# Performance work log

Hardware: AMD Instinct MI355X
Metric: run time of the kernel (lower is better)

Reference implementation:

```python
import jax, jax.numpy as jnp
import numpy as np

# Dimensions
T, B, N, E = 16, 16, 1024, 16384   # seq len, graphs per step, nodes/graph, edges/graph
F_IN, MID, H = 128, 16, 256        # node features, GCN mid channels, hidden_dim
RATIO = 0.8
K = int(np.ceil(RATIO * N))        # SAGPooling keeps K=820 nodes per graph


def setup_inputs() -> dict:
    key = jax.random.key(0)
    ks = jax.random.split(key, 16)
    def p(k, shape, s=0.05):
        return jax.random.normal(k, shape, dtype=jnp.float32) * s
    return {
        "x": jax.random.normal(ks[0], (T, B, N, F_IN), dtype=jnp.float32),
        "edge_index": jax.random.randint(ks[1], (T, B, 2, E), 0, N, dtype=jnp.int32),
        "conv1_W": p(ks[2], (F_IN, MID)),
        "conv1_b": p(ks[3], (MID,)),
        "sag_Wl": p(ks[4], (MID, 1)),   # GraphConv lin_rel (neighbor aggregate)
        "sag_Wr": p(ks[5], (MID, 1)),   # GraphConv lin_root (self)
        "sag_b": p(ks[6], (1,)),
        "conv2_W": p(ks[7], (MID, H)),
        "conv2_b": p(ks[8], (H,)),
        "W_ih": p(ks[9], (4 * H, H)),   # LSTM gates in PyTorch order i,f,g,o
        "W_hh": p(ks[10], (4 * H, H)),
        "b_ih": p(ks[11], (4 * H,)),
        "b_hh": p(ks[12], (4 * H,)),
        "cls_W": p(ks[13], (H, 1)),
        "cls_b": p(ks[14], (1,)),
    }


def _gcn(x, src, dst, w, W, b, n):
    # GCNConv with self-loops: out_i = sum_j d_i^-1/2 d_j^-1/2 w_ij (x_j W) + d_i^-1 (x_i W) + b
    h = x @ W                                            # [n, out]
    deg = jnp.ones((n,), x.dtype).at[dst].add(w)         # +1 for self-loop weight
    dinv = jax.lax.rsqrt(deg)
    coef = dinv[src] * dinv[dst] * w                     # [e]
    out = jnp.zeros_like(h).at[dst].add(h[src] * coef[:, None])
    return out + h * (dinv * dinv)[:, None] + b


def _graph_embed(x, ei, conv1_W, conv1_b, sag_Wl, sag_Wr, sag_b, conv2_W, conv2_b):
    src, dst = ei[0], ei[1]
    w = jnp.ones((E,), x.dtype)
    # conv1 + relu
    h1 = jax.nn.relu(_gcn(x, src, dst, w, conv1_W, conv1_b, N))
    # SAGPooling score via GraphConv(16 -> 1): sum-aggregate neighbors + root
    agg = jnp.zeros_like(h1).at[dst].add(h1[src])
    score = (agg @ sag_Wl + h1 @ sag_Wr + sag_b)[:, 0]   # [N]
    sv, perm = jax.lax.top_k(score, K)                   # top-k nodes
    xp = h1[perm] * jnp.tanh(sv)[:, None]                # gate kept nodes
    # remap edges to kept-node ids; drop edges touching removed nodes via zero weight
    newidx = jnp.full((N,), -1, jnp.int32).at[perm].set(jnp.arange(K, dtype=jnp.int32))
    ns, nd = newidx[src], newidx[dst]
    valid = (ns >= 0) & (nd >= 0)
    ew = valid.astype(x.dtype)
    ns = jnp.where(valid, ns, 0)
    nd = jnp.where(valid, nd, 0)
    # conv2 + relu, then global mean pool over the K kept nodes
    h2 = jax.nn.relu(_gcn(xp, ns, nd, ew, conv2_W, conv2_b, K))
    return h2.mean(axis=0)                               # [H]


def reference(x, edge_index, conv1_W, conv1_b, sag_Wl, sag_Wr, sag_b,
              conv2_W, conv2_b, W_ih, W_hh, b_ih, b_hh, cls_W, cls_b):
    embed = lambda xg, eg: _graph_embed(xg, eg, conv1_W, conv1_b,
                                        sag_Wl, sag_Wr, sag_b, conv2_W, conv2_b)
    emb = jax.vmap(jax.vmap(embed))(x, edge_index)       # [T, B, H]

    def step(carry, xt):
        h, c = carry
        g = xt @ W_ih.T + b_ih + h @ W_hh.T + b_hh
        i, f, gg, o = jnp.split(g, 4, axis=-1)
        c = jax.nn.sigmoid(f) * c + jax.nn.sigmoid(i) * jnp.tanh(gg)
        h = jax.nn.sigmoid(o) * jnp.tanh(c)
        return (h, c), None

    h0 = jnp.zeros((B, H), x.dtype)
    (hT, _), _ = jax.lax.scan(step, (h0, h0), emb)       # hT = lstm_out[:, -1, :]
    return hT @ cls_W + cls_b                            # [B, 1]
```

## Files before the change

### kernel.cpp

```cpp
#include <hip/hip_runtime.h>
#include <cmath>

#define TT 16
#define BB 16
#define NN 1024
#define EE 16384
#define FIN 128
#define MIDC 16
#define HH 256
#define KK 820
#define HS 20

#define OFF_HBUF   0
#define N_HBUF     (NN*HS)
#define OFF_CSR    (OFF_HBUF + N_HBUF)
#define N_CSR      (EE/2)
#define OFF_HEAD   (OFF_CSR + N_CSR)
#define OFF_CUR    (OFF_HEAD + NN + 1)
#define OFF_SCANA  (OFF_CUR + NN)
#define OFF_DINV   (OFF_SCANA + NN)
#define OFF_UB     (OFF_DINV + NN)
#define OFF_HIST   (OFF_UB + NN)
#define OFF_S      (OFF_HIST + 256)
#define OFF_WCNT   (OFF_S + 256)
#define OFF_CTRL   (OFF_WCNT + 16)
#define SM_FLOATS  (OFF_CTRL + 8)
#define SM_BYTES   (SM_FLOATS * 4)

__global__ __launch_bounds__(1024) void k_graph(
    const float* __restrict__ x, const int* __restrict__ ei,
    const float* __restrict__ W1, const float* __restrict__ b1,
    const float* __restrict__ Wl, const float* __restrict__ Wr,
    const float* __restrict__ bsag, const float* __restrict__ W2,
    const float* __restrict__ b2, float* __restrict__ emb)
{
  extern __shared__ __align__(16) float sm[];
  float*          hbuf  = sm + OFF_HBUF;
  float4*         hb4   = (float4*)hbuf;
  unsigned short* csr   = (unsigned short*)(sm + OFF_CSR);
  int*            head  = (int*)(sm + OFF_HEAD);
  int*            cur   = (int*)(sm + OFF_CUR);
  float*          dinvb = sm + OFF_DINV;
  unsigned*       ubv   = (unsigned*)(sm + OFF_UB);
  int*            hist  = (int*)(sm + OFF_HIST);
  int*            S     = (int*)(sm + OFF_S);
  int*            wcnt  = (int*)(sm + OFF_WCNT);
  int*            ctrl  = (int*)(sm + OFF_CTRL);

  const int g   = blockIdx.x;
  const int tid = threadIdx.x;
  const float* xg   = x  + (size_t)g * (NN*FIN);
  const int*   srcp = ei + (size_t)g * (2*EE);
  const int*   dstp = srcp + EE;

  cur[tid] = 0;

  float hown[MIDC];
  {
    const float4* xr = (const float4*)(xg + (size_t)tid * FIN);
#pragma unroll
    for (int c = 0; c < MIDC; ++c) hown[c] = 0.0f;
    for (int k4 = 0; k4 < FIN/4; ++k4) {
      float4 v = xr[k4];
      const float* w0 = W1 + (k4*4 + 0)*MIDC;
      const float* w1 = W1 + (k4*4 + 1)*MIDC;
      const float* w2 = W1 + (k4*4 + 2)*MIDC;
      const float* w3 = W1 + (k4*4 + 3)*MIDC;
#pragma unroll
      for (int c = 0; c < MIDC; ++c)
        hown[c] += v.x*w0[c] + v.y*w1[c] + v.z*w2[c] + v.w*w3[c];
    }
    hb4[tid*5+0] = make_float4(hown[0],  hown[1],  hown[2],  hown[3]);
    hb4[tid*5+1] = make_float4(hown[4],  hown[5],  hown[6],  hown[7]);
    hb4[tid*5+2] = make_float4(hown[8],  hown[9],  hown[10], hown[11]);
    hb4[tid*5+3] = make_float4(hown[12], hown[13], hown[14], hown[15]);
  }
  __syncthreads();

  for (int e = tid; e < EE; e += 1024) atomicAdd(&cur[dstp[e]], 1);
  __syncthreads();

  {
    const int lane_ = tid & 63, wid_ = tid >> 6;
    int v = cur[tid];
    int xscan = v;
#pragma unroll
    for (int off = 1; off < 64; off <<= 1) {
      int y = __shfl_up(xscan, off);
      if (lane_ >= off) xscan += y;
    }
    if (lane_ == 63) wcnt[wid_] = xscan;
    __syncthreads();
    if (tid < 64) {
      int w = (tid < 16) ? wcnt[tid] : 0;
#pragma unroll
      for (int off = 1; off < 16; off <<= 1) {
        int y = __shfl_up(w, off);
        if (tid >= off) w += y;
      }
      if (tid < 16) wcnt[tid] = w;
    }
    __syncthreads();
    int ex = xscan - v + ((wid_ == 0) ? 0 : wcnt[wid_ - 1]);
    head[tid] = ex;
    cur[tid]  = ex;
    if (tid == 0) head[NN] = EE;
    dinvb[tid] = rsqrtf((float)(v + 1));
  }
  __syncthreads();

  for (int e = tid; e < EE; e += 1024) {
    int s = srcp[e], d = dstp[e];
    int pos = atomicAdd(&cur[d], 1);
    csr[pos] = (unsigned short)s;
  }
  __syncthreads();

  const int beg = head[tid], end = head[tid+1];

  float h1own[MIDC];
  {
    float accv[MIDC];
#pragma unroll
    for (int c = 0; c < MIDC; ++c) accv[c] = 0.0f;
    for (int p = beg; p < end; ++p) {
      int s = csr[p];
      float ds_ = dinvb[s];
      float4 a0 = hb4[s*5+0], a1 = hb4[s*5+1], a2 = hb4[s*5+2], a3 = hb4[s*5+3];
      accv[0]  += a0.x*ds_; accv[1]  += a0.y*ds_; accv[2]  += a0.z*ds_; accv[3]  += a0.w*ds_;
      accv[4]  += a1.x*ds_; accv[5]  += a1.y*ds_; accv[6]  += a1.z*ds_; accv[7]  += a1.w*ds_;
      accv[8]  += a2.x*ds_; accv[9]  += a2.y*ds_; accv[10] += a2.z*ds_; accv[11] += a2.w*ds_;
      accv[12] += a3.x*ds_; accv[13] += a3.y*ds_; accv[14] += a3.z*ds_; accv[15] += a3.w*ds_;
    }
    float di = dinvb[tid];
#pragma unroll
    for (int c = 0; c < MIDC; ++c)
      h1own[c] = fmaxf(di*accv[c] + hown[c]*di*di + b1[c], 0.0f);
  }
  __syncthreads();
  hb4[tid*5+0] = make_float4(h1own[0],  h1own[1],  h1own[2],  h1own[3]);
  hb4[tid*5+1] = make_float4(h1own[4],  h1own[5],  h1own[6],  h1own[7]);
  hb4[tid*5+2] = make_float4(h1own[8],  h1own[9],  h1own[10], h1own[11]);
  hb4[tid*5+3] = make_float4(h1own[12], h1own[13], h1own[14], h1own[15]);
  __syncthreads();

  float score;
  unsigned myu;
  {
    float aggv[MIDC];
#pragma unroll
    for (int c = 0; c < MIDC; ++c) aggv[c] = 0.0f;
    for (int p = beg; p < end; ++p) {
      int s = csr[p];
      float4 a0 = hb4[s*5+0], a1 = hb4[s*5+1], a2 = hb4[s*5+2], a3 = hb4[s*5+3];
      aggv[0]  += a0.x; aggv[1]  += a0.y; aggv[2]  += a0.z; aggv[3]  += a0.w;
      aggv[4]  += a1.x; aggv[5]  += a1.y; aggv[6]  += a1.z; aggv[7]  += a1.w;
      aggv[8]  += a2.x; aggv[9]  += a2.y; aggv[10] += a2.z; aggv[11] += a2.w;
      aggv[12] += a3.x; aggv[13] += a3.y; aggv[14] += a3.z; aggv[15] += a3.w;
    }
    score = bsag[0];
#pragma unroll
    for (int c = 0; c < MIDC; ++c) score += aggv[c]*Wl[c] + h1own[c]*Wr[c];
    unsigned ubits = __float_as_uint(score);
    myu = (ubits & 0x80000000u) ? ~ubits : (ubits | 0x80000000u);
  }

  int remK = KK;
  unsigned pref = 0;
  for (int byte = 3; byte >= 0; --byte) {
    if (tid < 256) hist[tid] = 0;
    __syncthreads();
    const int sh = byte * 8;
    const unsigned hi_mask = (byte == 3) ? 0u : (0xFFFFFFFFu << (sh + 8));
    if ((myu & hi_mask) == pref) atomicAdd(&hist[(myu >> sh) & 255u], 1);
    __syncthreads();
    if (tid < 64) {
      int h0 = hist[tid*4+0], h1_ = hist[tid*4+1], h2_ = hist[tid*4+2], h3_ = hist[tid*4+3];
      int s3 = h3_, s2 = h2_ + s3, s1 = h1_ + s2, s0 = h0 + s1;
      int run = s0;
#pragma unroll
      for (int off = 1; off < 64; off <<= 1) {
        int o = __shfl_down(run, off);
        if (tid + off < 64) run += o;
      }
      int above = run - s0;
      S[tid*4+0] = above + s0;
      S[tid*4+1] = above + s1;
      S[tid*4+2] = above + s2;
      S[tid*4+3] = above + s3;
    }
    __syncthreads();
    if (tid < 256) {
      int Sv = S[tid];
      int Sn = (tid < 255) ? S[tid+1] : 0;
      if (Sv >= remK && Sn < remK) { ctrl[0] = remK - Sn; ctrl[1] = tid; }
    }
    __syncthreads();
    remK  = ctrl[0];
    pref |= ((unsigned)ctrl[1]) << sh;
    __syncthreads();
  }
  const unsigned vstar = pref;
  const int need = remK;

  {
    const int wid = tid >> 6, lane = tid & 63;
    bool eq = (myu == vstar);
    unsigned long long m = __ballot(eq);
    if (lane == 0) wcnt[wid] = __popcll(m);
    __syncthreads();
    int before = (lane == 0) ? 0 : __popcll(m & ((~0ull) >> (64 - lane)));
    for (int w = 0; w < wid; ++w) before += wcnt[w];
    int kept = (myu > vstar) ? 1 : (eq ? (before < need) : 0);
    float gate = kept ? tanhf(score) : 0.0f;
#pragma unroll
    for (int c = 0; c < MIDC; ++c) h1own[c] *= gate;
    hb4[tid*5+0] = make_float4(h1own[0],  h1own[1],  h1own[2],  h1own[3]);
    hb4[tid*5+1] = make_float4(h1own[4],  h1own[5],  h1own[6],  h1own[7]);
    hb4[tid*5+2] = make_float4(h1own[8],  h1own[9],  h1own[10], h1own[11]);
    hb4[tid*5+3] = make_float4(h1own[12], h1own[13], h1own[14], h1own[15]);
    ubv[tid] = (unsigned)kept;
  }
  __syncthreads();

  float di2;
  {
    int cnt2 = 0;
    for (int p = beg; p < end; ++p) cnt2 += (int)ubv[csr[p]];
    di2 = rsqrtf((float)(1 + cnt2));
    dinvb[tid] = di2;
  }
  __syncthreads();

  {
    float acc2[MIDC];
#pragma unroll
    for (int c = 0; c < MIDC; ++c) acc2[c] = 0.0f;
    for (int p = beg; p < end; ++p) {
      int s = csr[p];
      float ds_ = dinvb[s];
      float4 a0 = hb4[s*5+0], a1 = hb4[s*5+1], a2 = hb4[s*5+2], a3 = hb4[s*5+3];
      acc2[0]  += a0.x*ds_; acc2[1]  += a0.y*ds_; acc2[2]  += a0.z*ds_; acc2[3]  += a0.w*ds_;
      acc2[4]  += a1.x*ds_; acc2[5]  += a1.y*ds_; acc2[6]  += a1.z*ds_; acc2[7]  += a1.w*ds_;
      acc2[8]  += a2.x*ds_; acc2[9]  += a2.y*ds_; acc2[10] += a2.z*ds_; acc2[11] += a2.w*ds_;
      acc2[12] += a3.x*ds_; acc2[13] += a3.y*ds_; acc2[14] += a3.z*ds_; acc2[15] += a3.w*ds_;
    }
#pragma unroll
    for (int c = 0; c < MIDC; ++c)
      h1own[c] = di2*acc2[c] + h1own[c]*di2*di2;
  }
  __syncthreads();
  hb4[tid*5+0] = make_float4(h1own[0],  h1own[1],  h1own[2],  h1own[3]);
  hb4[tid*5+1] = make_float4(h1own[4],  h1own[5],  h1own[6],  h1own[7]);
  hb4[tid*5+2] = make_float4(h1own[8],  h1own[9],  h1own[10], h1own[11]);
  hb4[tid*5+3] = make_float4(h1own[12], h1own[13], h1own[14], h1own[15]);
  __syncthreads();

  {
    const int ig = tid >> 6, h4 = tid & 63;
    float4 w2c[MIDC];
#pragma unroll
    for (int c = 0; c < MIDC; ++c) w2c[c] = *(const float4*)(W2 + c*HH + (h4 << 2));
    float4 bv = *(const float4*)(b2 + (h4 << 2));
    float4 pacc = make_float4(0.f, 0.f, 0.f, 0.f);
    for (int k = 0; k < 64; ++k) {
      int i = (ig << 6) + k;
      if (ubv[i] == 0u) continue;
      float4 v0 = hb4[i*5+0], v1 = hb4[i*5+1], v2 = hb4[i*5+2], v3 = hb4[i*5+3];
      float vv[MIDC] = {v0.x,v0.y,v0.z,v0.w, v1.x,v1.y,v1.z,v1.w,
                        v2.x,v2.y,v2.z,v2.w, v3.x,v3.y,v3.z,v3.w};
      float t0 = bv.x, t1 = bv.y, t2 = bv.z, t3 = bv.w;
#pragma unroll
      for (int c = 0; c < MIDC; ++c) {
        t0 += vv[c]*w2c[c].x; t1 += vv[c]*w2c[c].y;
        t2 += vv[c]*w2c[c].z; t3 += vv[c]*w2c[c].w;
      }
      pacc.x += fmaxf(t0, 0.f); pacc.y += fmaxf(t1, 0.f);
      pacc.z += fmaxf(t2, 0.f); pacc.w += fmaxf(t3, 0.f);
    }
    float4* part4 = (float4*)(sm + OFF_CSR);
    part4[(ig << 6) + h4] = pacc;
  }
  __syncthreads();
  if (tid < HH) {
    const float* part = sm + OFF_CSR;
    float s = 0.f;
#pragma unroll
    for (int ig = 0; ig < 16; ++ig) s += part[ig*HH + tid];
    emb[(size_t)g*HH + tid] = s * (1.0f/(float)KK);
  }
}

__global__ __launch_bounds__(256) void k_lstm(
    const float* __restrict__ emb, const float* __restrict__ W_ih,
    const float* __restrict__ W_hh, const float* __restrict__ b_ih,
    const float* __restrict__ b_hh, const float* __restrict__ clsW,
    const float* __restrict__ clsb, float* __restrict__ hA,
    float* __restrict__ hB, int* __restrict__ flags, float* __restrict__ out)
{
  __shared__ __align__(16) float emb_s[16][HH];
  __shared__ __align__(16) float A_s[16][64];
  __shared__ __align__(16) float h_s[HH];
  __shared__ float gl[16][4];

  const int bid = blockIdx.x;
  const int b   = bid & 15, ug = bid >> 4;
  const int tid = threadIdx.x;
  const int ul  = tid >> 4, sub = tid & 15;
  const int u   = ug*16 + ul;

  for (int i = tid; i < 16*HH; i += 256) {
    int t = i >> 8, k = i & 255;
    emb_s[t][k] = emb[(size_t)(t*BB + b)*HH + k];
  }

  float4 wh[4][4];
#pragma unroll
  for (int g_ = 0; g_ < 4; ++g_) {
    const float4* wr = (const float4*)(W_hh + (size_t)(g_*HH + u)*HH);
    wh[g_][0] = wr[sub];      wh[g_][1] = wr[sub+16];
    wh[g_][2] = wr[sub+32];   wh[g_][3] = wr[sub+48];
  }
  __syncthreads();

#pragma unroll
  for (int g_ = 0; g_ < 4; ++g_) {
    const int j = g_*HH + u;
    const float4* wr = (const float4*)(W_ih + (size_t)j*HH);
    float4 w0 = wr[sub], w1 = wr[sub+16], w2 = wr[sub+32], w3 = wr[sub+48];
    float bj = b_ih[j] + b_hh[j];
    for (int t = 0; t < 16; ++t) {
      const float4* e4 = (const float4*)emb_s[t];
      float4 e0 = e4[sub], e1 = e4[sub+16], e2 = e4[sub+32], e3 = e4[sub+48];
      float p = w0.x*e0.x + w0.y*e0.y + w0.z*e0.z + w0.w*e0.w
              + w1.x*e1.x + w1.y*e1.y + w1.z*e1.z + w1.w*e1.w
              + w2.x*e2.x + w2.y*e2.y + w2.z*e2.z + w2.w*e2.w
              + w3.x*e3.x + w3.y*e3.y + w3.z*e3.z + w3.w*e3.w;
      p += __shfl_xor(p, 1); p += __shfl_xor(p, 2);
      p += __shfl_xor(p, 4); p += __shfl_xor(p, 8);
      if (sub == 0) A_s[t][g_*16 + ul] = p + bj;
    }
  }
  __syncthreads();

  float c = 0.0f;
  for (int s = 0; s < 16; ++s) {
    if (s == 0) {
      h_s[tid] = 0.0f;
    } else {
      const float* hr = (s & 1) ? hA : hB;
      h_s[tid] = __hip_atomic_load(&hr[b*HH + tid], __ATOMIC_RELAXED,
                                   __HIP_MEMORY_SCOPE_AGENT);
    }
    __syncthreads();

    const float4* h4 = (const float4*)h_s;
    float4 hv0 = h4[sub], hv1 = h4[sub+16], hv2 = h4[sub+32], hv3 = h4[sub+48];
    float gv[4];
#pragma unroll
    for (int g_ = 0; g_ < 4; ++g_) {
      float p = wh[g_][0].x*hv0.x + wh[g_][0].y*hv0.y + wh[g_][0].z*hv0.z + wh[g_][0].w*hv0.w
              + wh[g_][1].x*hv1.x + wh[g_][1].y*hv1.y + wh[g_][1].z*hv1.z + wh[g_][1].w*hv1.w
              + wh[g_][2].x*hv2.x + wh[g_][2].y*hv2.y + wh[g_][2].z*hv2.z + wh[g_][2].w*hv2.w
              + wh[g_][3].x*hv3.x + wh[g_][3].y*hv3.y + wh[g_][3].z*hv3.z + wh[g_][3].w*hv3.w;
      p += __shfl_xor(p, 1); p += __shfl_xor(p, 2);
      p += __shfl_xor(p, 4); p += __shfl_xor(p, 8);
      gv[g_] = p;
    }
    if (sub == 0) { gl[ul][0]=gv[0]; gl[ul][1]=gv[1]; gl[ul][2]=gv[2]; gl[ul][3]=gv[3]; }
    __syncthreads();

    if (tid < 16) {
      float gi = gl[tid][0] + A_s[s][     tid];
      float gf = gl[tid][1] + A_s[s][16 + tid];
      float gn = gl[tid][2] + A_s[s][32 + tid];
      float go = gl[tid][3] + A_s[s][48 + tid];
      float iv = 1.0f/(1.0f + expf(-gi));
      float fv = 1.0f/(1.0f + expf(-gf));
      float gg = tanhf(gn);
      float ov = 1.0f/(1.0f + expf(-go));
      c = fv*c + iv*gg;
      float hv = ov * tanhf(c);
      float* hw = (s & 1) ? hB : hA;
      __hip_atomic_store(&hw[b*HH + ug*16 + tid], hv, __ATOMIC_RELAXED,
                         __HIP_MEMORY_SCOPE_AGENT);
      if (s == 15) {
        float p = hv * clsW[ug*16 + tid];
        p += __shfl_xor(p, 1); p += __shfl_xor(p, 2);
        p += __shfl_xor(p, 4); p += __shfl_xor(p, 8);
        if (tid == 0) atomicAdd(&out[b], p + (ug == 0 ? clsb[0] : 0.0f));
      }
    }

    if (s < 15) {
      __syncthreads();
      if (tid == 0)
        __hip_atomic_store(&flags[(b << 4) + ug], s + 1, __ATOMIC_RELAXED,
                           __HIP_MEMORY_SCOPE_AGENT);
      if (tid < 64) {
        const int target = s + 1;
        for (;;) {
          int fv = __hip_atomic_load(&flags[(b << 4) + (tid & 15)],
                                     __ATOMIC_RELAXED, __HIP_MEMORY_SCOPE_AGENT);
          if (__all(fv >= target)) break;
          __builtin_amdgcn_s_sleep(1);
        }
      }
      __syncthreads();
    }
  }
}

extern "C" void kernel_launch(void* const* d_in, const int* in_sizes, int n_in,
                              void* d_out, int out_size, void* d_ws, size_t ws_size,
                              hipStream_t stream)
{
  const float* x    = (const float*)d_in[0];
  const int*   ei   = (const int*)  d_in[1];
  const float* W1   = (const float*)d_in[2];
  const float* b1   = (const float*)d_in[3];
  const float* Wl   = (const float*)d_in[4];
  const float* Wr   = (const float*)d_in[5];
  const float* bs   = (const float*)d_in[6];
  const float* W2   = (const float*)d_in[7];
  const float* b2   = (const float*)d_in[8];
  const float* Wih  = (const float*)d_in[9];
  const float* Whh  = (const float*)d_in[10];
  const float* bih  = (const float*)d_in[11];
  const float* bhh  = (const float*)d_in[12];
  const float* clsW = (const float*)d_in[13];
  const float* clsb = (const float*)d_in[14];
  float* out = (float*)d_out;

  float* emb   = (float*)d_ws;
  float* hA    = emb + (size_t)TT*BB*HH;
  float* hB    = hA + BB*HH;
  int*   flags = (int*)(hB + BB*HH);

  (void)hipFuncSetAttribute(reinterpret_cast<const void*>(k_graph),
      hipFuncAttributeMaxDynamicSharedMemorySize, SM_BYTES);

  hipLaunchKernelGGL(k_graph, dim3(TT*BB), dim3(1024), SM_BYTES, stream,
                     x, ei, W1, b1, Wl, Wr, bs, W2, b2, emb);
  (void)hipMemsetAsync(flags, 0, BB*BB*sizeof(int), stream);
  (void)hipMemsetAsync(out, 0, BB*sizeof(float), stream);
  hipLaunchKernelGGL(k_lstm, dim3(256), dim3(256), 0, stream,
                     emb, Wih, Whh, bih, bhh, clsW, clsb, hA, hB, flags, out);
}
```

Baseline: 391.0 us.

## Precompute SAG projection, prefetch CSR gathers, and use per-step sentinel handoff in LSTM

The SAG score aggregation now projects each node's h1 onto Wl before aggregating, so the neighbor loop sums one float per edge instead of sixteen. Both GCN aggregation loops software-prefetch the next neighbor's features to hide LDS latency. The LSTM drops its flag barrier and instead stores each step's hidden state in a separate buffer initialised to a -1 sentinel, which readers spin on. This removes a block-wide sync and flag round trip per step, but adds a larger memset and relies on no real hidden value having the sentinel bit pattern.

Measured after the change: 386.8 us. About the same (-1.1%).

```diff
diff --git a/kernel.cpp b/kernel.cpp
--- a/kernel.cpp
+++ b/kernel.cpp
@@ -40,6 +40,7 @@
   unsigned short* csr   = (unsigned short*)(sm + OFF_CSR);
   int*            head  = (int*)(sm + OFF_HEAD);
   int*            cur   = (int*)(sm + OFF_CUR);
+  float*          qbuf  = sm + OFF_SCANA;
   float*          dinvb = sm + OFF_DINV;
   unsigned*       ubv   = (unsigned*)(sm + OFF_UB);
   int*            hist  = (int*)(sm + OFF_HIST);
@@ -123,14 +124,23 @@
     float accv[MIDC];
 #pragma unroll
     for (int c = 0; c < MIDC; ++c) accv[c] = 0.0f;
-    for (int p = beg; p < end; ++p) {
-      int s = csr[p];
-      float ds_ = dinvb[s];
-      float4 a0 = hb4[s*5+0], a1 = hb4[s*5+1], a2 = hb4[s*5+2], a3 = hb4[s*5+3];
-      accv[0]  += a0.x*ds_; accv[1]  += a0.y*ds_; accv[2]  += a0.z*ds_; accv[3]  += a0.w*ds_;
-      accv[4]  += a1.x*ds_; accv[5]  += a1.y*ds_; accv[6]  += a1.z*ds_; accv[7]  += a1.w*ds_;
-      accv[8]  += a2.x*ds_; accv[9]  += a2.y*ds_; accv[10] += a2.z*ds_; accv[11] += a2.w*ds_;
-      accv[12] += a3.x*ds_; accv[13] += a3.y*ds_; accv[14] += a3.z*ds_; accv[15] += a3.w*ds_;
+    if (beg < end) {
+      int sC = csr[beg];
+      float4 a0 = hb4[sC*5+0], a1 = hb4[sC*5+1], a2 = hb4[sC*5+2], a3 = hb4[sC*5+3];
+      float dsC = dinvb[sC];
+      for (int p = beg; p < end; ++p) {
+        float4 b0 = a0, b1 = a1, b2 = a2, b3 = a3;
+        float dsB = dsC;
+        if (p + 1 < end) {
+          int sN = csr[p+1];
+          a0 = hb4[sN*5+0]; a1 = hb4[sN*5+1]; a2 = hb4[sN*5+2]; a3 = hb4[sN*5+3];
+          dsC = dinvb[sN];
+        }
+        accv[0]  += b0.x*dsB; accv[1]  += b0.y*dsB; accv[2]  += b0.z*dsB; accv[3]  += b0.w*dsB;
+        accv[4]  += b1.x*dsB; accv[5]  += b1.y*dsB; accv[6]  += b1.z*dsB; accv[7]  += b1.w*dsB;
+        accv[8]  += b2.x*dsB; accv[9]  += b2.y*dsB; accv[10] += b2.z*dsB; accv[11] += b2.w*dsB;
+        accv[12] += b3.x*dsB; accv[13] += b3.y*dsB; accv[14] += b3.z*dsB; accv[15] += b3.w*dsB;
+      }
     }
     float di = dinvb[tid];
 #pragma unroll
@@ -142,25 +152,22 @@
   hb4[tid*5+1] = make_float4(h1own[4],  h1own[5],  h1own[6],  h1own[7]);
   hb4[tid*5+2] = make_float4(h1own[8],  h1own[9],  h1own[10], h1own[11]);
   hb4[tid*5+3] = make_float4(h1own[12], h1own[13], h1own[14], h1own[15]);
+  {
+    float q = 0.0f;
+#pragma unroll
+    for (int c = 0; c < MIDC; ++c) q += h1own[c]*Wl[c];
+    qbuf[tid] = q;
+  }
   __syncthreads();
 
   float score;
   unsigned myu;
   {
-    float aggv[MIDC];
-#pragma unroll
-    for (int c = 0; c < MIDC; ++c) aggv[c] = 0.0f;
-    for (int p = beg; p < end; ++p) {
-      int s = csr[p];
-      float4 a0 = hb4[s*5+0], a1 = hb4[s*5+1], a2 = hb4[s*5+2], a3 = hb4[s*5+3];
-      aggv[0]  += a0.x; aggv[1]  += a0.y; aggv[2]  += a0.z; aggv[3]  += a0.w;
-      aggv[4]  += a1.x; aggv[5]  += a1.y; aggv[6]  += a1.z; aggv[7]  += a1.w;
-      aggv[8]  += a2.x; aggv[9]  += a2.y; aggv[10] += a2.z; aggv[11] += a2.w;
-      aggv[12] += a3.x; aggv[13] += a3.y; aggv[14] += a3.z; aggv[15] += a3.w;
-    }
-    score = bsag[0];
-#pragma unroll
-    for (int c = 0; c < MIDC; ++c) score += aggv[c]*Wl[c] + h1own[c]*Wr[c];
+    float qsum = 0.0f;
+    for (int p = beg; p < end; ++p) qsum += qbuf[csr[p]];
+    score = bsag[0] + qsum;
+#pragma unroll
+    for (int c = 0; c < MIDC; ++c) score += h1own[c]*Wr[c];
     unsigned ubits = __float_as_uint(score);
     myu = (ubits & 0x80000000u) ? ~ubits : (ubits | 0x80000000u);
   }
@@ -236,14 +243,23 @@
     float acc2[MIDC];
 #pragma unroll
     for (int c = 0; c < MIDC; ++c) acc2[c] = 0.0f;
-    for (int p = beg; p < end; ++p) {
-      int s = csr[p];
-      float ds_ = dinvb[s];
-      float4 a0 = hb4[s*5+0], a1 = hb4[s*5+1], a2 = hb4[s*5+2], a3 = hb4[s*5+3];
-      acc2[0]  += a0.x*ds_; acc2[1]  += a0.y*ds_; acc2[2]  += a0.z*ds_; acc2[3]  += a0.w*ds_;
-      acc2[4]  += a1.x*ds_; acc2[5]  += a1.y*ds_; acc2[6]  += a1.z*ds_; acc2[7]  += a1.w*ds_;
-      acc2[8]  += a2.x*ds_; acc2[9]  += a2.y*ds_; acc2[10] += a2.z*ds_; acc2[11] += a2.w*ds_;
-      acc2[12] += a3.x*ds_; acc2[13] += a3.y*ds_; acc2[14] += a3.z*ds_; acc2[15] += a3.w*ds_;
+    if (beg < end) {
+      int sC = csr[beg];
+      float4 a0 = hb4[sC*5+0], a1 = hb4[sC*5+1], a2 = hb4[sC*5+2], a3 = hb4[sC*5+3];
+      float dsC = dinvb[sC];
+      for (int p = beg; p < end; ++p) {
+        float4 b0 = a0, b1 = a1, b2 = a2, b3 = a3;
+        float dsB = dsC;
+        if (p + 1 < end) {
+          int sN = csr[p+1];
+          a0 = hb4[sN*5+0]; a1 = hb4[sN*5+1]; a2 = hb4[sN*5+2]; a3 = hb4[sN*5+3];
+          dsC = dinvb[sN];
+        }
+        acc2[0]  += b0.x*dsB; acc2[1]  += b0.y*dsB; acc2[2]  += b0.z*dsB; acc2[3]  += b0.w*dsB;
+        acc2[4]  += b1.x*dsB; acc2[5]  += b1.y*dsB; acc2[6]  += b1.z*dsB; acc2[7]  += b1.w*dsB;
+        acc2[8]  += b2.x*dsB; acc2[9]  += b2.y*dsB; acc2[10] += b2.z*dsB; acc2[11] += b2.w*dsB;
+        acc2[12] += b3.x*dsB; acc2[13] += b3.y*dsB; acc2[14] += b3.z*dsB; acc2[15] += b3.w*dsB;
+      }
     }
 #pragma unroll
     for (int c = 0; c < MIDC; ++c)
@@ -295,8 +311,8 @@
     const float* __restrict__ emb, const float* __restrict__ W_ih,
     const float* __restrict__ W_hh, const float* __restrict__ b_ih,
     const float* __restrict__ b_hh, const float* __restrict__ clsW,
-    const float* __restrict__ clsb, float* __restrict__ hA,
-    float* __restrict__ hB, int* __restrict__ flags, float* __restrict__ out)
+    const float* __restrict__ clsb, int* __restrict__ hstep,
+    float* __restrict__ out)
 {
   __shared__ __align__(16) float emb_s[16][HH];
   __shared__ __align__(16) float A_s[16][64];
@@ -348,9 +364,15 @@
     if (s == 0) {
       h_s[tid] = 0.0f;
     } else {
-      const float* hr = (s & 1) ? hA : hB;
-      h_s[tid] = __hip_atomic_load(&hr[b*HH + tid], __ATOMIC_RELAXED,
-                                   __HIP_MEMORY_SCOPE_AGENT);
+      const int* src = hstep + ((size_t)(s-1)*BB + b)*HH;
+      int v = __hip_atomic_load(&src[tid], __ATOMIC_RELAXED,
+                                __HIP_MEMORY_SCOPE_AGENT);
+      while (v == -1) {
+        __builtin_amdgcn_s_sleep(1);
+        v = __hip_atomic_load(&src[tid], __ATOMIC_RELAXED,
+                              __HIP_MEMORY_SCOPE_AGENT);
+      }
+      h_s[tid] = __int_as_float(v);
     }
     __syncthreads();
 
@@ -381,32 +403,16 @@
       float ov = 1.0f/(1.0f + expf(-go));
       c = fv*c + iv*gg;
       float hv = ov * tanhf(c);
-      float* hw = (s & 1) ? hB : hA;
-      __hip_atomic_store(&hw[b*HH + ug*16 + tid], hv, __ATOMIC_RELAXED,
-                         __HIP_MEMORY_SCOPE_AGENT);
-      if (s == 15) {
+      if (s < 15) {
+        __hip_atomic_store(&hstep[((size_t)s*BB + b)*HH + ug*16 + tid],
+                           __float_as_int(hv), __ATOMIC_RELAXED,
+                           __HIP_MEMORY_SCOPE_AGENT);
+      } else {
         float p = hv * clsW[ug*16 + tid];
         p += __shfl_xor(p, 1); p += __shfl_xor(p, 2);
         p += __shfl_xor(p, 4); p += __shfl_xor(p, 8);
         if (tid == 0) atomicAdd(&out[b], p + (ug == 0 ? clsb[0] : 0.0f));
       }
-    }
-
-    if (s < 15) {
-      __syncthreads();
-      if (tid == 0)
-        __hip_atomic_store(&flags[(b << 4) + ug], s + 1, __ATOMIC_RELAXED,
-                           __HIP_MEMORY_SCOPE_AGENT);
-      if (tid < 64) {
-        const int target = s + 1;
-        for (;;) {
-          int fv = __hip_atomic_load(&flags[(b << 4) + (tid & 15)],
-                                     __ATOMIC_RELAXED, __HIP_MEMORY_SCOPE_AGENT);
-          if (__all(fv >= target)) break;
-          __builtin_amdgcn_s_sleep(1);
-        }
-      }
-      __syncthreads();
     }
   }
 }
@@ -433,17 +439,15 @@
   float* out = (float*)d_out;
 
   float* emb   = (float*)d_ws;
-  float* hA    = emb + (size_t)TT*BB*HH;
-  float* hB    = hA + BB*HH;
-  int*   flags = (int*)(hB + BB*HH);
+  int*   hstep = (int*)(emb + (size_t)TT*BB*HH);
 
   (void)hipFuncSetAttribute(reinterpret_cast<const void*>(k_graph),
       hipFuncAttributeMaxDynamicSharedMemorySize, SM_BYTES);
 
   hipLaunchKernelGGL(k_graph, dim3(TT*BB), dim3(1024), SM_BYTES, stream,
                      x, ei, W1, b1, Wl, Wr, bs, W2, b2, emb);
-  (void)hipMemsetAsync(flags, 0, BB*BB*sizeof(int), stream);
+  (void)hipMemsetAsync(hstep, 0xFF, (size_t)15*BB*HH*sizeof(int), stream);
   (void)hipMemsetAsync(out, 0, BB*sizeof(float), stream);
   hipLaunchKernelGGL(k_lstm, dim3(256), dim3(256), 0, stream,
-                     emb, Wih, Whh, bih, bhh, clsW, clsb, hA, hB, flags, out);
+                     emb, Wih, Whh, bih, bhh, clsW, clsb, hstep, out);
 }
```
